# Kernel optimization log

Hardware: AMD Instinct MI355X
Metric: run time of the kernel (lower is better)

The kernel has to match this reference:

```python
import jax, jax.numpy as jnp
import numpy as np

T, N, K = 32, 1024, 15
IN_CH, CONV_CH, HEADS, ODIM = 64, 64, 2, 50
D = CONV_CH // 2  # GRU hidden size (conv_ch // 2)


def setup_inputs():
    ks = jax.random.split(jax.random.key(0), 24)
    x = jax.random.normal(ks[0], (T, N, IN_CH), jnp.float32)
    # fixed-degree adjacency: exactly K distinct non-self sources per (t, target)
    rnd = jax.random.uniform(ks[1], (T, N, N - 1))
    off = jnp.argsort(rnd, axis=-1)[..., :K]            # [T,N,K] in [0, N-2]
    tgt = jnp.arange(N)[None, :, None]
    src = (tgt + 1 + off) % N                           # distinct sources != target
    edge = jnp.zeros((T, N, N), jnp.int32).at[jnp.arange(T)[:, None, None], src, tgt].set(1)

    def lin(k, fi, fo):
        return jax.random.normal(k, (fi, fo), jnp.float32) / float(np.sqrt(fi))

    p, i = {}, 2
    for nm, fi, c in (("g1", IN_CH, CONV_CH), ("g2", CONV_CH, D), ("r1", D, CONV_CH), ("f1", D, CONV_CH)):
        p[nm + "_Wl"] = lin(ks[i], fi, HEADS * c)
        p[nm + "_bl"] = jnp.zeros((HEADS * c,), jnp.float32)
        p[nm + "_Wr"] = lin(ks[i + 1], fi, HEADS * c)
        p[nm + "_br"] = jnp.zeros((HEADS * c,), jnp.float32)
        p[nm + "_att"] = jax.random.normal(ks[i + 2], (HEADS, c), jnp.float32) / float(np.sqrt(c))
        p[nm + "_b"] = jnp.zeros((c,), jnp.float32)
        i += 3
    for nm in ("gru0", "gru1"):
        p[nm + "_Wih"] = lin(ks[i], D, 3 * D).T         # [3D, D], PyTorch layout
        p[nm + "_Whh"] = lin(ks[i + 1], D, 3 * D).T
        p[nm + "_bih"] = jnp.zeros((3 * D,), jnp.float32)
        p[nm + "_bhh"] = jnp.zeros((3 * D,), jnp.float32)
        i += 2
    p["rec2_W"] = lin(ks[i], CONV_CH, IN_CH)
    p["rec2_b"] = jnp.zeros((IN_CH,), jnp.float32)
    p["rec3_W"] = lin(ks[i + 1], IN_CH, ODIM)
    p["rec3_b"] = jnp.zeros((ODIM,), jnp.float32)
    p["fore3_W"] = lin(ks[i + 2], IN_CH, ODIM)
    p["fore3_b"] = jnp.zeros((ODIM,), jnp.float32)
    return {"x": x, "edge": edge, **p}


def _gat(x, srcs, prm):
    # GATv2Conv, concat=False: mean over heads; srcs: [K+1, N] sources per target
    Wl, bl, Wr, br, att, bias = prm
    H, C = att.shape
    gl = (x @ Wl + bl).reshape(-1, H, C)                # source-side lin_l
    gr = (x @ Wr + br).reshape(-1, H, C)                # target-side lin_r
    gsrc = gl[srcs]                                     # [K+1, N, H, C] gather
    e = jax.nn.leaky_relu(gsrc + gr[None], 0.2)
    logits = jnp.einsum('knhc,hc->knh', e, att)
    alpha = jax.nn.softmax(logits, axis=0)              # softmax over neighbors per target
    return jnp.einsum('knh,knhc->nhc', alpha, gsrc).mean(axis=1) + bias


def _gat_t(xs, srcs, prm):
    return jax.vmap(lambda a, s: _gat(a, s, prm))(xs, srcs)


def _gru(xs, Wih, Whh, bih, bhh):
    # PyTorch GRU cell math, zero initial state, seq-first [T, N, D]
    h0 = jnp.zeros((xs.shape[1], Whh.shape[1]), xs.dtype)

    def step(h, xt):
        gi = xt @ Wih.T + bih
        gh = h @ Whh.T + bhh
        ir, iz, inew = jnp.split(gi, 3, axis=-1)
        hr, hz, hn = jnp.split(gh, 3, axis=-1)
        r = jax.nn.sigmoid(ir + hr)
        z = jax.nn.sigmoid(iz + hz)
        n = jnp.tanh(inew + r * hn)
        hnew = (1.0 - z) * n + z * h
        return hnew, hnew

    _, ys = jax.lax.scan(step, h0, xs)
    return ys


def _forward(x, edge, g1, g2, r1, f1, gru0, gru1, rec2_W, rec2_b, rec3_W, rec3_b, fore3_W, fore3_b):
    # recover the K in-edges per target (edge[t, src, tgt] == 1), then append self loops
    srcs = jnp.argsort(-edge, axis=1)[:, :K, :]         # [T, K, N]
    self_idx = jnp.broadcast_to(jnp.arange(N)[None, None, :], (edge.shape[0], 1, N))
    srcs = jnp.concatenate([srcs, self_idx.astype(srcs.dtype)], axis=1)  # [T, K+1, N]

    out = jax.nn.elu(_gat_t(x, srcs, g1))               # dropout is a no-op in eval
    out2 = jax.nn.elu(_gat_t(out, srcs, g2))
    E = _gru(out2, *gru0)
    E = _gru(E, *gru1)

    rec = jax.nn.elu(_gat_t(E[1:], srcs[1:], r1))       # timesteps 1..T-1
    rec = jnp.tanh(rec @ rec2_W + rec2_b)
    recon = rec @ rec3_W + rec3_b

    fc = jax.nn.elu(_gat_t(E[:-1], srcs[:-1], f1))      # timesteps 0..T-2
    fc = jnp.tanh(fc @ rec2_W + rec2_b)                 # original code reuses reconstruct2 here
    forecast = fc @ fore3_W + fore3_b
    return recon, forecast, E


def reference(x, edge, g1_Wl, g1_bl, g1_Wr, g1_br, g1_att, g1_b,
              g2_Wl, g2_bl, g2_Wr, g2_br, g2_att, g2_b,
              r1_Wl, r1_bl, r1_Wr, r1_br, r1_att, r1_b,
              f1_Wl, f1_bl, f1_Wr, f1_br, f1_att, f1_b,
              gru0_Wih, gru0_Whh, gru0_bih, gru0_bhh,
              gru1_Wih, gru1_Whh, gru1_bih, gru1_bhh,
              rec2_W, rec2_b, rec3_W, rec3_b, fore3_W, fore3_b):
    return _forward(x, edge,
                    (g1_Wl, g1_bl, g1_Wr, g1_br, g1_att, g1_b),
                    (g2_Wl, g2_bl, g2_Wr, g2_br, g2_att, g2_b),
                    (r1_Wl, r1_bl, r1_Wr, r1_br, r1_att, r1_b),
                    (f1_Wl, f1_bl, f1_Wr, f1_br, f1_att, f1_b),
                    (gru0_Wih, gru0_Whh, gru0_bih, gru0_bhh),
                    (gru1_Wih, gru1_Whh, gru1_bih, gru1_bhh),
                    rec2_W, rec2_b, rec3_W, rec3_b, fore3_W, fore3_b)
```

## Files before the change

### kernel.cpp

```cpp
#include <hip/hip_runtime.h>
#include <math.h>

static constexpr int Tt = 32;
static constexpr int Nn = 1024;
static constexpr int KN = 16;

template <int M>
__device__ __forceinline__ float lane_xor(float v) {
    if constexpr (M == 1)
        return __int_as_float(__builtin_amdgcn_mov_dpp(__float_as_int(v), 0xB1, 0xF, 0xF, true));
    else if constexpr (M == 2)
        return __int_as_float(__builtin_amdgcn_mov_dpp(__float_as_int(v), 0x4E, 0xF, 0xF, true));
    else
        return __shfl_xor(v, M);
}
__device__ __forceinline__ float bcastlane(float v, int l) {
    return __int_as_float(__builtin_amdgcn_readlane(__float_as_int(v), l));
}
__device__ __forceinline__ constexpr int rev4(int k) {
    return ((k & 1) << 3) | ((k & 2) << 1) | ((k & 4) >> 1) | ((k & 8) >> 3);
}
template <int NV, int M>
__device__ __forceinline__ void fstage(float* p, int lane) {
#pragma unroll
    for (int k2 = 0; k2 < NV / 2; ++k2) {
        float a_ = p[k2], b_ = p[k2 + NV / 2];
        float t_ = (lane & M) ? a_ : b_;
        float r_ = lane_xor<M>(t_);
        p[k2] = ((lane & M) ? b_ : a_) + r_;
    }
}
__device__ __forceinline__ float fold16(float* p, int lane) {
    fstage<16, 1>(p, lane); fstage<8, 2>(p, lane);
    fstage<4, 4>(p, lane);  fstage<2, 8>(p, lane);
    return p[0];
}
__device__ __forceinline__ float rmax16(float x) {
    x = fmaxf(x, lane_xor<1>(x)); x = fmaxf(x, lane_xor<2>(x));
    x = fmaxf(x, lane_xor<4>(x)); x = fmaxf(x, lane_xor<8>(x));
    return x;
}
__device__ __forceinline__ float rsum16(float x) {
    x += lane_xor<1>(x); x += lane_xor<2>(x);
    x += lane_xor<4>(x); x += lane_xor<8>(x);
    return x;
}

__global__ __launch_bounds__(1024) void k_srcs(const int* __restrict__ edge,
                                               int* __restrict__ srcs)
{
    __shared__ int cnt[128];
    const int t    = blockIdx.x >> 3;
    const int tgt0 = (blockIdx.x & 7) << 7;
    const int x = threadIdx.x & 31;
    const int y = threadIdx.x >> 5;
    if (threadIdx.x < 128) cnt[threadIdx.x] = 0;
    __syncthreads();

    const int c0 = 4 * x;
    const int s0 = y * 32;
    const int* e = edge + (size_t)t * Nn * Nn + tgt0 + c0;

    for (int i0 = 0; i0 < 32; i0 += 8) {
        int4 v[8];
#pragma unroll
        for (int j = 0; j < 8; ++j)
            v[j] = *reinterpret_cast<const int4*>(e + (size_t)(s0 + i0 + j) * Nn);
#pragma unroll
        for (int j = 0; j < 8; ++j) {
            const int s = s0 + i0 + j;
            if (v[j].x) { int sl = atomicAdd(&cnt[c0],     1); if (sl < KN - 1) srcs[((size_t)t * Nn + tgt0 + c0)     * KN + sl] = s; }
            if (v[j].y) { int sl = atomicAdd(&cnt[c0 + 1], 1); if (sl < KN - 1) srcs[((size_t)t * Nn + tgt0 + c0 + 1) * KN + sl] = s; }
            if (v[j].z) { int sl = atomicAdd(&cnt[c0 + 2], 1); if (sl < KN - 1) srcs[((size_t)t * Nn + tgt0 + c0 + 2) * KN + sl] = s; }
            if (v[j].w) { int sl = atomicAdd(&cnt[c0 + 3], 1); if (sl < KN - 1) srcs[((size_t)t * Nn + tgt0 + c0 + 3) * KN + sl] = s; }
        }
    }
    if (threadIdx.x < 128)
        srcs[((size_t)t * Nn + tgt0 + threadIdx.x) * KN + (KN - 1)] = tgt0 + threadIdx.x;
}

template <int FI, int FO>
__global__ __launch_bounds__(256) void k_lin2t(
    const float* __restrict__ X,
    const float* __restrict__ Wl, const float* __restrict__ bl,
    const float* __restrict__ Wr, const float* __restrict__ br,
    float* __restrict__ Yl, float* __restrict__ Yr, int rows)
{
    constexpr int HC = FO / 2;
    constexpr int RG = 256 / HC;
    constexpr int R  = 8;
    constexpr int BR = RG * R;
    constexpr int F4 = FI / 4;
    __shared__ float xs[BR][FI];

    const int tid  = threadIdx.x;
    const int c    = tid % HC;
    const int g    = tid / HC;
    const int row0 = blockIdx.x * BR;

#pragma unroll
    for (int idx = tid; idx < BR * F4; idx += 256) {
        int r = idx / F4, q = idx % F4;
        reinterpret_cast<float4*>(&xs[r][0])[q] =
            reinterpret_cast<const float4*>(X + (size_t)(row0 + r) * FI)[q];
    }
    __syncthreads();

    float al0[R], al1[R], ar0[R], ar1[R];
    const float bl0 = bl[c], bl1 = bl[c + HC], br0 = br[c], br1 = br[c + HC];
#pragma unroll
    for (int r = 0; r < R; ++r) { al0[r] = bl0; al1[r] = bl1; ar0[r] = br0; ar1[r] = br1; }

    const int rb = g * R;
#pragma unroll
    for (int i0 = 0; i0 < FI; i0 += 4) {
        float4 xv[R];
#pragma unroll
        for (int r = 0; r < R; ++r)
            xv[r] = *reinterpret_cast<const float4*>(&xs[rb + r][i0]);
#pragma unroll
        for (int j = 0; j < 4; ++j) {
            const float wl0 = Wl[(i0 + j) * FO + c];
            const float wl1 = Wl[(i0 + j) * FO + c + HC];
            const float wr0 = Wr[(i0 + j) * FO + c];
            const float wr1 = Wr[(i0 + j) * FO + c + HC];
#pragma unroll
            for (int r = 0; r < R; ++r) {
                const float xx = (&xv[r].x)[j];
                al0[r] = fmaf(xx, wl0, al0[r]);
                al1[r] = fmaf(xx, wl1, al1[r]);
                ar0[r] = fmaf(xx, wr0, ar0[r]);
                ar1[r] = fmaf(xx, wr1, ar1[r]);
            }
        }
    }
#pragma unroll
    for (int r = 0; r < R; ++r) {
        const size_t ro = (size_t)(row0 + rb + r) * FO;
        reinterpret_cast<float2*>(Yl + ro)[c] = make_float2(al0[r], al1[r]);
        reinterpret_cast<float2*>(Yr + ro)[c] = make_float2(ar0[r], ar1[r]);
    }
}

__global__ __launch_bounds__(256) void k_lin2td(
    const float* __restrict__ E,
    const float* __restrict__ WlA, const float* __restrict__ blA,
    const float* __restrict__ WrA, const float* __restrict__ brA,
    float* __restrict__ YlA, float* __restrict__ YrA,
    const float* __restrict__ WlB, const float* __restrict__ blB,
    const float* __restrict__ WrB, const float* __restrict__ brB,
    float* __restrict__ YlB, float* __restrict__ YrB)
{
    constexpr int FI = 32, FO = 128, HC = 64, R = 8, BR = 32, F4 = FI / 4;
    __shared__ float xs[BR][FI];

    int bid = blockIdx.x;
    const bool second = bid >= 992;
    if (second) bid -= 992;

    const float* X  = second ? E   : (E + (size_t)Nn * FI);
    const float* Wl = second ? WlB : WlA;
    const float* bl = second ? blB : blA;
    const float* Wr = second ? WrB : WrA;
    const float* br = second ? brB : brA;
    float* Yl = second ? YlB : YlA;
    float* Yr = second ? YrB : YrA;

    const int tid  = threadIdx.x;
    const int c    = tid % HC;
    const int g    = tid / HC;
    const int row0 = bid * BR;

#pragma unroll
    for (int idx = tid; idx < BR * F4; idx += 256) {
        int r = idx / F4, q = idx % F4;
        reinterpret_cast<float4*>(&xs[r][0])[q] =
            reinterpret_cast<const float4*>(X + (size_t)(row0 + r) * FI)[q];
    }
    __syncthreads();

    float al0[R], al1[R], ar0[R], ar1[R];
    const float bl0 = bl[c], bl1 = bl[c + HC], br0 = br[c], br1 = br[c + HC];
#pragma unroll
    for (int r = 0; r < R; ++r) { al0[r] = bl0; al1[r] = bl1; ar0[r] = br0; ar1[r] = br1; }

    const int rb = g * R;
#pragma unroll
    for (int i0 = 0; i0 < FI; i0 += 4) {
        float4 xv[R];
#pragma unroll
        for (int r = 0; r < R; ++r)
            xv[r] = *reinterpret_cast<const float4*>(&xs[rb + r][i0]);
#pragma unroll
        for (int j = 0; j < 4; ++j) {
            const float wl0 = Wl[(i0 + j) * FO + c];
            const float wl1 = Wl[(i0 + j) * FO + c + HC];
            const float wr0 = Wr[(i0 + j) * FO + c];
            const float wr1 = Wr[(i0 + j) * FO + c + HC];
#pragma unroll
            for (int r = 0; r < R; ++r) {
                const float xx = (&xv[r].x)[j];
                al0[r] = fmaf(xx, wl0, al0[r]);
                al1[r] = fmaf(xx, wl1, al1[r]);
                ar0[r] = fmaf(xx, wr0, ar0[r]);
                ar1[r] = fmaf(xx, wr1, ar1[r]);
            }
        }
    }
#pragma unroll
    for (int r = 0; r < R; ++r) {
        const size_t ro = (size_t)(row0 + rb + r) * FO;
        reinterpret_cast<float2*>(Yl + ro)[c] = make_float2(al0[r], al1[r]);
        reinterpret_cast<float2*>(Yr + ro)[c] = make_float2(ar0[r], ar1[r]);
    }
}

__global__ __launch_bounds__(192) void k_lin96(
    const float* __restrict__ X, const float* __restrict__ W,
    const float* __restrict__ b, float* __restrict__ Y)
{
    __shared__ float wT[32 * 97];
    __shared__ float xs[16][32];

    const int tid = threadIdx.y * 96 + threadIdx.x;
    const int row0 = blockIdx.x * 16;

    for (int idx = tid; idx < 3072; idx += 192) {
        int c = idx >> 5, i = idx & 31;
        wT[i * 97 + c] = W[idx];
    }
    for (int idx = tid; idx < 128; idx += 192)
        reinterpret_cast<float4*>(xs)[idx] =
            reinterpret_cast<const float4*>(X + (size_t)row0 * 32)[idx];
    __syncthreads();

    const int c  = threadIdx.x;
    const int rb = threadIdx.y * 8;
    float acc[8];
    const float bc = b[c];
#pragma unroll
    for (int r = 0; r < 8; ++r) acc[r] = bc;

#pragma unroll
    for (int i = 0; i < 32; ++i) {
        const float w = wT[i * 97 + c];
#pragma unroll
        for (int r = 0; r < 8; ++r)
            acc[r] = fmaf(xs[rb + r][i], w, acc[r]);
    }
#pragma unroll
    for (int r = 0; r < 8; ++r)
        Y[(size_t)(row0 + rb + r) * 96 + c] = acc[r];
}

__global__ __launch_bounds__(64) void k_gru1(
    const float* __restrict__ gi, const float* __restrict__ Whh,
    const float* __restrict__ bhh, float* __restrict__ E)
{
    const int d    = threadIdx.x & 31;
    const int node = blockIdx.x * 2 + (threadIdx.x >> 5);

    float wr_[32], wz_[32], wn_[32];
#pragma unroll
    for (int q = 0; q < 8; ++q) {
        *reinterpret_cast<float4*>(&wr_[q * 4]) =
            reinterpret_cast<const float4*>(Whh + (size_t)d * 32)[q];
        *reinterpret_cast<float4*>(&wz_[q * 4]) =
            reinterpret_cast<const float4*>(Whh + (size_t)(32 + d) * 32)[q];
        *reinterpret_cast<float4*>(&wn_[q * 4]) =
            reinterpret_cast<const float4*>(Whh + (size_t)(64 + d) * 32)[q];
    }
    const float br_ = bhh[d], bz_ = bhh[32 + d], bn_ = bhh[64 + d];

    size_t base = (size_t)node * 96 + d;
    float gr = gi[base], gz = gi[base + 32], gn = gi[base + 64];

    float h = 0.0f;
    for (int t = 0; t < Tt; ++t) {
        float grn = 0.f, gzn = 0.f, gnn = 0.f;
        if (t < Tt - 1) {
            const size_t nb = ((size_t)(t + 1) * Nn + node) * 96 + d;
            grn = gi[nb]; gzn = gi[nb + 32]; gnn = gi[nb + 64];
        }
        float ar = br_, az = bz_, an = bn_;
#pragma unroll
        for (int i = 0; i < 32; ++i) {
            const float hv = __shfl(h, i, 32);
            ar = fmaf(wr_[i], hv, ar);
            az = fmaf(wz_[i], hv, az);
            an = fmaf(wn_[i], hv, an);
        }
        const float r = __builtin_amdgcn_rcpf(1.0f + expf(-(gr + ar)));
        const float z = __builtin_amdgcn_rcpf(1.0f + expf(-(gz + az)));
        const float nn2 = tanhf(gn + r * an);
        h = (1.0f - z) * nn2 + z * h;
        E[((size_t)t * Nn + node) * 32 + d] = h;
        gr = grn; gz = gzn; gn = gnn;
    }
}

__device__ __forceinline__ float gat64_body(
    const float* __restrict__ gl, const float* __restrict__ gr,
    const int* __restrict__ srcs, const float* __restrict__ att,
    const float* __restrict__ bias, int wave, int lane)
{
    const int t = wave >> 10;
    const int n = wave & (Nn - 1);

    const float2 grl = reinterpret_cast<const float2*>(gr + (size_t)wave * 128)[lane];
    const float a0 = att[lane], a1 = att[64 + lane];

    const int4* sp = reinterpret_cast<const int4*>(srcs + ((size_t)t * Nn + n) * KN);
    const int4 sA = sp[0], sB = sp[1], sC = sp[2], sD = sp[3];
    int s[KN] = {sA.x, sA.y, sA.z, sA.w, sB.x, sB.y, sB.z, sB.w,
                 sC.x, sC.y, sC.z, sC.w, sD.x, sD.y, sD.z, sD.w};

    const float2* glt = reinterpret_cast<const float2*>(gl) + ((size_t)t * Nn * 64);

    float2 g[KN];
    float p0[KN], p1[KN];
#pragma unroll
    for (int k = 0; k < KN; ++k) {
        g[k] = glt[(unsigned)((s[k] << 6) | lane)];
        float e0 = g[k].x + grl.x; e0 = fmaxf(e0, 0.2f * e0);
        float e1 = g[k].y + grl.y; e1 = fmaxf(e1, 0.2f * e1);
        p0[k] = e0 * a0; p1[k] = e1 * a1;
    }
    float lo0 = fold16(p0, lane);
    lo0 += lane_xor<16>(lo0); lo0 += __shfl_xor(lo0, 32);
    float lo1 = fold16(p1, lane);
    lo1 += lane_xor<16>(lo1); lo1 += __shfl_xor(lo1, 32);

    const float m0 = rmax16(lo0), m1 = rmax16(lo1);
    const float e0 = expf(lo0 - m0), e1 = expf(lo1 - m1);
    const float A0 = e0 * __builtin_amdgcn_rcpf(rsum16(e0));
    const float A1 = e1 * __builtin_amdgcn_rcpf(rsum16(e1));

    float acc0 = 0.0f, acc1 = 0.0f;
#pragma unroll
    for (int k = 0; k < KN; ++k) {
        acc0 = fmaf(bcastlane(A0, rev4(k)), g[k].x, acc0);
        acc1 = fmaf(bcastlane(A1, rev4(k)), g[k].y, acc1);
    }
    float res = 0.5f * (acc0 + acc1) + bias[lane];
    return res > 0.0f ? res : expm1f(res);
}

__global__ __launch_bounds__(256, 4) void k_gat64(
    const float* __restrict__ gl, const float* __restrict__ gr,
    const int* __restrict__ srcs, const float* __restrict__ att,
    const float* __restrict__ bias, float* __restrict__ out, int rows)
{
    const int lane = threadIdx.x & 63;
    const int w = threadIdx.x >> 6;
    const int gridB = rows >> 2;
    const int chunk = gridB >> 3;
    const int bid = blockIdx.x;
    const int lb = (bid & 7) * chunk + (bid >> 3);
    const int wave = lb * 4 + w;
    const float res = gat64_body(gl, gr, srcs, att, bias, wave, lane);
    out[(size_t)wave * 64 + lane] = res;
}

__global__ __launch_bounds__(256, 4) void k_gat64h2(
    const float* __restrict__ glA, const float* __restrict__ grA,
    const int* __restrict__ srcsA, const float* __restrict__ attA,
    const float* __restrict__ biasA, float* __restrict__ outA,
    const float* __restrict__ W3A, const float* __restrict__ b3A,
    const float* __restrict__ glB, const float* __restrict__ grB,
    const int* __restrict__ srcsB, const float* __restrict__ attB,
    const float* __restrict__ biasB, float* __restrict__ outB,
    const float* __restrict__ W3B, const float* __restrict__ b3B,
    const float* __restrict__ W2, const float* __restrict__ b2)
{
    __shared__ float hb[4][64];
    constexpr int rows = (Tt - 1) * Nn;
    constexpr int gridH = rows >> 2;
    constexpr int chunk = gridH >> 3;

    int bid = blockIdx.x;
    const bool second = bid >= gridH;
    if (second) bid -= gridH;

    const float* gl   = second ? glB   : glA;
    const float* gr   = second ? grB   : grA;
    const int*   srcs = second ? srcsB : srcsA;
    const float* att  = second ? attB  : attA;
    const float* bias = second ? biasB : biasA;
    float*       out  = second ? outB  : outA;
    const float* W3   = second ? W3B   : W3A;
    const float* b3   = second ? b3B   : b3A;

    const int lane = threadIdx.x & 63;
    const int w = threadIdx.x >> 6;
    const int lb = (bid & 7) * chunk + (bid >> 3);
    const int wave = lb * 4 + w;

    const float res = gat64_body(gl, gr, srcs, att, bias, wave, lane);

    hb[w][lane] = res;
    float acc = b2[lane];
#pragma unroll
    for (int i4 = 0; i4 < 16; ++i4) {
        const float4 hv = reinterpret_cast<const float4*>(&hb[w][0])[i4];
        acc = fmaf(hv.x, W2[(i4 * 4 + 0) * 64 + lane], acc);
        acc = fmaf(hv.y, W2[(i4 * 4 + 1) * 64 + lane], acc);
        acc = fmaf(hv.z, W2[(i4 * 4 + 2) * 64 + lane], acc);
        acc = fmaf(hv.w, W2[(i4 * 4 + 3) * 64 + lane], acc);
    }
    const float th = tanhf(acc);
    hb[w][lane] = th;
    if (lane < 50) {
        float a = b3[lane];
#pragma unroll
        for (int j4 = 0; j4 < 16; ++j4) {
            const float4 hv = reinterpret_cast<const float4*>(&hb[w][0])[j4];
            a = fmaf(hv.x, W3[(j4 * 4 + 0) * 50 + lane], a);
            a = fmaf(hv.y, W3[(j4 * 4 + 1) * 50 + lane], a);
            a = fmaf(hv.z, W3[(j4 * 4 + 2) * 50 + lane], a);
            a = fmaf(hv.w, W3[(j4 * 4 + 3) * 50 + lane], a);
        }
        out[(size_t)wave * 50 + lane] = a;
    }
}

__global__ __launch_bounds__(256, 4) void k_gat32(
    const float* __restrict__ gl, const float* __restrict__ gr,
    const int* __restrict__ srcs, const float* __restrict__ att,
    const float* __restrict__ bias, float* __restrict__ out, int waves)
{
    const int lane = threadIdx.x & 63;
    const int w = threadIdx.x >> 6;
    const int gridB = waves >> 2;
    const int chunk = gridB >> 3;
    const int bid = blockIdx.x;
    const int lb = (bid & 7) * chunk + (bid >> 3);
    const int wv = lb * 4 + w;
    const int tgt = 2 * wv + (lane >> 5);
    const int t = tgt >> 10;
    const int n = tgt & (Nn - 1);
    const int c = lane & 31;

    const float2 grl = reinterpret_cast<const float2*>(gr + (size_t)tgt * 64)[c];
    const float a0 = att[c], a1 = att[32 + c];

    const int4* sp = reinterpret_cast<const int4*>(srcs + ((size_t)t * Nn + n) * KN);
    const int4 sA = sp[0], sB = sp[1], sC = sp[2], sD = sp[3];
    int s[KN] = {sA.x, sA.y, sA.z, sA.w, sB.x, sB.y, sB.z, sB.w,
                 sC.x, sC.y, sC.z, sC.w, sD.x, sD.y, sD.z, sD.w};

    const float2* glt = reinterpret_cast<const float2*>(gl) + ((size_t)t * Nn * 32);

    float2 g[KN];
    float p0[KN], p1[KN];
#pragma unroll
    for (int k = 0; k < KN; ++k) {
        g[k] = glt[(unsigned)((s[k] << 5) | c)];
        float e0 = g[k].x + grl.x; e0 = fmaxf(e0, 0.2f * e0);
        float e1 = g[k].y + grl.y; e1 = fmaxf(e1, 0.2f * e1);
        p0[k] = e0 * a0; p1[k] = e1 * a1;
    }
    float lo0 = fold16(p0, lane); lo0 += lane_xor<16>(lo0);
    float lo1 = fold16(p1, lane); lo1 += lane_xor<16>(lo1);

    const float m0 = rmax16(lo0), m1 = rmax16(lo1);
    const float e0 = expf(lo0 - m0), e1 = expf(lo1 - m1);
    const float A0 = e0 * __builtin_amdgcn_rcpf(rsum16(e0));
    const float A1 = e1 * __builtin_amdgcn_rcpf(rsum16(e1));

    const float A0o = __shfl_xor(A0, 32);
    const float A1o = __shfl_xor(A1, 32);
    const bool loHalf = (lane < 32);

    float acc0 = 0.0f, acc1 = 0.0f;
#pragma unroll
    for (int k = 0; k < KN; ++k) {
        const float b0a = bcastlane(A0, rev4(k)), b0b = bcastlane(A0o, rev4(k));
        const float b1a = bcastlane(A1, rev4(k)), b1b = bcastlane(A1o, rev4(k));
        acc0 = fmaf(loHalf ? b0a : b0b, g[k].x, acc0);
        acc1 = fmaf(loHalf ? b1a : b1b, g[k].y, acc1);
    }
    float res = 0.5f * (acc0 + acc1) + bias[c];
    res = res > 0.0f ? res : expm1f(res);
    out[(size_t)tgt * 32 + c] = res;
}

extern "C" void kernel_launch(void* const* d_in, const int* in_sizes, int n_in,
                              void* d_out, int out_size, void* d_ws, size_t ws_size,
                              hipStream_t stream)
{
    const float* x    = (const float*)d_in[0];
    const int*   edge = (const int*)d_in[1];

    const float *g1_Wl = (const float*)d_in[2],  *g1_bl = (const float*)d_in[3];
    const float *g1_Wr = (const float*)d_in[4],  *g1_br = (const float*)d_in[5];
    const float *g1_att= (const float*)d_in[6],  *g1_b  = (const float*)d_in[7];
    const float *g2_Wl = (const float*)d_in[8],  *g2_bl = (const float*)d_in[9];
    const float *g2_Wr = (const float*)d_in[10], *g2_br = (const float*)d_in[11];
    const float *g2_att= (const float*)d_in[12], *g2_b  = (const float*)d_in[13];
    const float *r1_Wl = (const float*)d_in[14], *r1_bl = (const float*)d_in[15];
    const float *r1_Wr = (const float*)d_in[16], *r1_br = (const float*)d_in[17];
    const float *r1_att= (const float*)d_in[18], *r1_b  = (const float*)d_in[19];
    const float *f1_Wl = (const float*)d_in[20], *f1_bl = (const float*)d_in[21];
    const float *f1_Wr = (const float*)d_in[22], *f1_br = (const float*)d_in[23];
    const float *f1_att= (const float*)d_in[24], *f1_b  = (const float*)d_in[25];
    const float *gru0_Wih = (const float*)d_in[26], *gru0_Whh = (const float*)d_in[27];
    const float *gru0_bih = (const float*)d_in[28], *gru0_bhh = (const float*)d_in[29];
    const float *gru1_Wih = (const float*)d_in[30], *gru1_Whh = (const float*)d_in[31];
    const float *gru1_bih = (const float*)d_in[32], *gru1_bhh = (const float*)d_in[33];
    const float *rec2_W = (const float*)d_in[34], *rec2_b = (const float*)d_in[35];
    const float *rec3_W = (const float*)d_in[36], *rec3_b = (const float*)d_in[37];
    const float *fore3_W= (const float*)d_in[38], *fore3_b= (const float*)d_in[39];

    char* ws = (char*)d_ws;
    int*   srcs = (int*)ws;
    float* buf1 = (float*)(ws + (4u << 20));
    float* buf2 = buf1 + (size_t)32768 * 128;
    float* buf3 = buf2 + (size_t)32768 * 128;
    float* buf4 = buf3 + (size_t)32768 * 128;
    float* buf5 = buf4 + (size_t)32768 * 128;
    float* buf6 = buf5 + (size_t)32768 * 64;

    float* recon = (float*)d_out;
    float* fore  = recon + (size_t)31 * 1024 * 50;
    float* E     = fore  + (size_t)31 * 1024 * 50;

    k_srcs<<<Tt * 8, 1024, 0, stream>>>(edge, srcs);

    k_lin2t<64, 128><<<1024, 256, 0, stream>>>(x, g1_Wl, g1_bl, g1_Wr, g1_br, buf1, buf2, 32768);
    k_gat64<<<8192, 256, 0, stream>>>(buf1, buf2, srcs, g1_att, g1_b, buf5, 32768);

    k_lin2t<64, 64><<<512, 256, 0, stream>>>(buf5, g2_Wl, g2_bl, g2_Wr, g2_br, buf1, buf2, 32768);
    k_gat32<<<4096, 256, 0, stream>>>(buf1, buf2, srcs, g2_att, g2_b, buf6, 16384);

    k_lin96<<<2048, dim3(96, 2), 0, stream>>>(buf6, gru0_Wih, gru0_bih, buf1);
    k_gru1<<<512, 64, 0, stream>>>(buf1, gru0_Whh, gru0_bhh, buf5);
    k_lin96<<<2048, dim3(96, 2), 0, stream>>>(buf5, gru1_Wih, gru1_bih, buf2);
    k_gru1<<<512, 64, 0, stream>>>(buf2, gru1_Whh, gru1_bhh, E);

    k_lin2td<<<1984, 256, 0, stream>>>(E,
        r1_Wl, r1_bl, r1_Wr, r1_br, buf1, buf2,
        f1_Wl, f1_bl, f1_Wr, f1_br, buf3, buf4);

    k_gat64h2<<<15872, 256, 0, stream>>>(
        buf1, buf2, srcs + (size_t)KN * Nn, r1_att, r1_b, recon, rec3_W, rec3_b,
        buf3, buf4, srcs,                   f1_att, f1_b, fore,  fore3_W, fore3_b,
        rec2_W, rec2_b);

    (void)in_sizes; (void)n_in; (void)out_size; (void)ws_size;
}
```

Measured before the change: 288.2 us.

## Split fused GAT+head kernel into two GAT launches and a row-tiled head kernel

Replaces the fused kernel that ran the reconstruct/forecast GAT layers together with their per-wave 64x64 and 64x50 MLP heads. It now runs two plain GAT launches that write intermediates to workspace, then a separate head kernel. That kernel tiles 32 rows per block in shared memory and reuses each weight load across 8 rows per thread. The aim is to stop reloading W2/W3 once per row and to lighten register and LDS pressure in the GAT kernel, at the cost of an extra round trip of intermediates through global memory and two more launches.

```diff
diff --git a/kernel.cpp b/kernel.cpp
--- a/kernel.cpp
+++ b/kernel.cpp
@@ -362,68 +362,6 @@
     out[(size_t)wave * 64 + lane] = res;
 }
 
-__global__ __launch_bounds__(256, 4) void k_gat64h2(
-    const float* __restrict__ glA, const float* __restrict__ grA,
-    const int* __restrict__ srcsA, const float* __restrict__ attA,
-    const float* __restrict__ biasA, float* __restrict__ outA,
-    const float* __restrict__ W3A, const float* __restrict__ b3A,
-    const float* __restrict__ glB, const float* __restrict__ grB,
-    const int* __restrict__ srcsB, const float* __restrict__ attB,
-    const float* __restrict__ biasB, float* __restrict__ outB,
-    const float* __restrict__ W3B, const float* __restrict__ b3B,
-    const float* __restrict__ W2, const float* __restrict__ b2)
-{
-    __shared__ float hb[4][64];
-    constexpr int rows = (Tt - 1) * Nn;
-    constexpr int gridH = rows >> 2;
-    constexpr int chunk = gridH >> 3;
-
-    int bid = blockIdx.x;
-    const bool second = bid >= gridH;
-    if (second) bid -= gridH;
-
-    const float* gl   = second ? glB   : glA;
-    const float* gr   = second ? grB   : grA;
-    const int*   srcs = second ? srcsB : srcsA;
-    const float* att  = second ? attB  : attA;
-    const float* bias = second ? biasB : biasA;
-    float*       out  = second ? outB  : outA;
-    const float* W3   = second ? W3B   : W3A;
-    const float* b3   = second ? b3B   : b3A;
-
-    const int lane = threadIdx.x & 63;
-    const int w = threadIdx.x >> 6;
-    const int lb = (bid & 7) * chunk + (bid >> 3);
-    const int wave = lb * 4 + w;
-
-    const float res = gat64_body(gl, gr, srcs, att, bias, wave, lane);
-
-    hb[w][lane] = res;
-    float acc = b2[lane];
-#pragma unroll
-    for (int i4 = 0; i4 < 16; ++i4) {
-        const float4 hv = reinterpret_cast<const float4*>(&hb[w][0])[i4];
-        acc = fmaf(hv.x, W2[(i4 * 4 + 0) * 64 + lane], acc);
-        acc = fmaf(hv.y, W2[(i4 * 4 + 1) * 64 + lane], acc);
-        acc = fmaf(hv.z, W2[(i4 * 4 + 2) * 64 + lane], acc);
-        acc = fmaf(hv.w, W2[(i4 * 4 + 3) * 64 + lane], acc);
-    }
-    const float th = tanhf(acc);
-    hb[w][lane] = th;
-    if (lane < 50) {
-        float a = b3[lane];
-#pragma unroll
-        for (int j4 = 0; j4 < 16; ++j4) {
-            const float4 hv = reinterpret_cast<const float4*>(&hb[w][0])[j4];
-            a = fmaf(hv.x, W3[(j4 * 4 + 0) * 50 + lane], a);
-            a = fmaf(hv.y, W3[(j4 * 4 + 1) * 50 + lane], a);
-            a = fmaf(hv.z, W3[(j4 * 4 + 2) * 50 + lane], a);
-            a = fmaf(hv.w, W3[(j4 * 4 + 3) * 50 + lane], a);
-        }
-        out[(size_t)wave * 50 + lane] = a;
-    }
-}
-
 __global__ __launch_bounds__(256, 4) void k_gat32(
     const float* __restrict__ gl, const float* __restrict__ gr,
     const int* __restrict__ srcs, const float* __restrict__ att,
@@ -483,6 +421,71 @@
     float res = 0.5f * (acc0 + acc1) + bias[c];
     res = res > 0.0f ? res : expm1f(res);
     out[(size_t)tgt * 32 + c] = res;
+}
+
+__global__ __launch_bounds__(256) void k_head2(
+    const float* __restrict__ inA, const float* __restrict__ W3A,
+    const float* __restrict__ b3A, float* __restrict__ outA,
+    const float* __restrict__ inB, const float* __restrict__ W3B,
+    const float* __restrict__ b3B, float* __restrict__ outB,
+    const float* __restrict__ W2, const float* __restrict__ b2)
+{
+    __shared__ float xs[32][64];
+    __shared__ float tmp[32][64];
+
+    int bid = blockIdx.x;
+    const bool second = bid >= 992;
+    if (second) bid -= 992;
+
+    const float* in  = second ? inB  : inA;
+    const float* W3  = second ? W3B  : W3A;
+    const float* b3  = second ? b3B  : b3A;
+    float*       out = second ? outB : outA;
+
+    const int c = threadIdx.x;
+    const int g = threadIdx.y;
+    const int tid = g * 64 + c;
+    const int row0 = bid * 32;
+
+    for (int idx = tid; idx < 32 * 16; idx += 256) {
+        int r = idx >> 4, q = idx & 15;
+        reinterpret_cast<float4*>(&xs[r][0])[q] =
+            reinterpret_cast<const float4*>(in + (size_t)(row0 + r) * 64)[q];
+    }
+    __syncthreads();
+
+    const int rb = g * 8;
+    float acc[8];
+    const float bc = b2[c];
+#pragma unroll
+    for (int r = 0; r < 8; ++r) acc[r] = bc;
+#pragma unroll
+    for (int i = 0; i < 64; ++i) {
+        const float w2 = W2[i * 64 + c];
+#pragma unroll
+        for (int r = 0; r < 8; ++r)
+            acc[r] = fmaf(xs[rb + r][i], w2, acc[r]);
+    }
+#pragma unroll
+    for (int r = 0; r < 8; ++r) tmp[rb + r][c] = tanhf(acc[r]);
+
+    const int cc = c < 50 ? c : 0;
+    float a[8];
+    const float b3c = b3[cc];
+#pragma unroll
+    for (int r = 0; r < 8; ++r) a[r] = b3c;
+#pragma unroll
+    for (int j = 0; j < 64; ++j) {
+        const float w3 = W3[j * 50 + cc];
+#pragma unroll
+        for (int r = 0; r < 8; ++r)
+            a[r] = fmaf(tmp[rb + r][j], w3, a[r]);
+    }
+    if (c < 50) {
+#pragma unroll
+        for (int r = 0; r < 8; ++r)
+            out[(size_t)(row0 + rb + r) * 50 + c] = a[r];
+    }
 }
 
 extern "C" void kernel_launch(void* const* d_in, const int* in_sizes, int n_in,
@@ -542,9 +545,11 @@
         r1_Wl, r1_bl, r1_Wr, r1_br, buf1, buf2,
         f1_Wl, f1_bl, f1_Wr, f1_br, buf3, buf4);
 
-    k_gat64h2<<<15872, 256, 0, stream>>>(
-        buf1, buf2, srcs + (size_t)KN * Nn, r1_att, r1_b, recon, rec3_W, rec3_b,
-        buf3, buf4, srcs,                   f1_att, f1_b, fore,  fore3_W, fore3_b,
+    k_gat64<<<7936, 256, 0, stream>>>(buf1, buf2, srcs + (size_t)KN * Nn, r1_att, r1_b, buf5, 31744);
+    k_gat64<<<7936, 256, 0, stream>>>(buf3, buf4, srcs, f1_att, f1_b, buf1, 31744);
+    k_head2<<<1984, dim3(64, 4), 0, stream>>>(
+        buf5, rec3_W, rec3_b, recon,
+        buf1, fore3_W, fore3_b, fore,
         rec2_W, rec2_b);
 
     (void)in_sizes; (void)n_in; (void)out_size; (void)ws_size;
```

Result: no change. 290.2 us (+0.7%).
